# Optimization experiments

Measured on AMD Instinct MI355X. Metric: run time of the kernel, lower is better.

Reference implementation:

```python
import jax, jax.numpy as jnp
import numpy as np


def setup_inputs() -> dict:
    key = jax.random.key(0)
    k1, k2 = jax.random.split(key)
    B, Q, K, H = 8, 2048, 2048, 128
    out_state = jax.random.normal(k1, (B, Q, H), dtype=jnp.float32)
    history = jax.random.normal(k2, (B, K, H), dtype=jnp.float32)
    return {"out_state": out_state, "history": history}


def reference(out_state, history):
    # tanh pre-activation on queries
    q = jnp.tanh(out_state)                              # [B, Q, H]
    # unscaled QK^T scores
    scores = jnp.einsum("bqh,bkh->bqk", q, history)      # [B, Q, K]
    probs = jax.nn.softmax(scores, axis=2)               # softmax over keys
    attn = jnp.einsum("bqk,bkh->bqh", probs, history)    # [B, Q, H]
    return attn
```

## Files before the change

### kernel.cpp

```cpp
#include <hip/hip_runtime.h>
#include <math.h>


typedef _Float16 half8 __attribute__((ext_vector_type(8)));
typedef _Float16 half4 __attribute__((ext_vector_type(4)));
typedef float    f32x4 __attribute__((ext_vector_type(4)));

#define QQ 2048
#define KK 2048
#define HH 128
#define BM 128
#define BN 64
#define NTILES 32
#define NGROUPS 128
#define KS_STR 132
#define VT_STR 68
#define PS_STR 66
#define L2E 1.44269504f
#define SPLITS_MAX 6
#define OSPLIT  ((size_t)NGROUPS * BM * HH)
#define MLSPLIT ((size_t)NGROUPS * BM)

union U32H { unsigned int u; _Float16 h[2]; };

__launch_bounds__(256, 3)
__global__ void attn_main(const float* __restrict__ out_state,
                          const float* __restrict__ history,
                          float* __restrict__ out,
                          float* __restrict__ ws,
                          int splits) {
    __shared__ _Float16 Ks[BN * KS_STR];
    __shared__ _Float16 Vt[HH * VT_STR];
    __shared__ _Float16 Ps[4][2][16 * PS_STR];

    const int tid  = threadIdx.x;
    const int wave = tid >> 6;
    const int lane = tid & 63;
    const int quad = lane >> 4;
    const int lc   = lane & 15;

    const int bid = blockIdx.x;
    const int b   = bid & 7;
    const int t   = bid >> 3;
    const int qb  = t & 15;
    const int s   = t >> 4;
    const int g   = b * 16 + qb;
    const int m0  = qb * BM;

    const int kt0 = (NTILES * s) / splits;
    const int kt1 = (NTILES * (s + 1)) / splits;

    half8 qfa[4], qfb[4];
    {
        const float* qrowA = out_state + ((size_t)b * QQ + m0 + wave * 32 + lc) * HH;
        const float* qrowB = qrowA + 16 * HH;
        #pragma unroll
        for (int s4 = 0; s4 < 4; ++s4) {
            const int h0 = 32 * s4 + quad * 8;
            float4 a = *(const float4*)(qrowA + h0);
            float4 c = *(const float4*)(qrowA + h0 + 4);
            qfa[s4][0] = (_Float16)tanhf(a.x); qfa[s4][1] = (_Float16)tanhf(a.y);
            qfa[s4][2] = (_Float16)tanhf(a.z); qfa[s4][3] = (_Float16)tanhf(a.w);
            qfa[s4][4] = (_Float16)tanhf(c.x); qfa[s4][5] = (_Float16)tanhf(c.y);
            qfa[s4][6] = (_Float16)tanhf(c.z); qfa[s4][7] = (_Float16)tanhf(c.w);
            a = *(const float4*)(qrowB + h0);
            c = *(const float4*)(qrowB + h0 + 4);
            qfb[s4][0] = (_Float16)tanhf(a.x); qfb[s4][1] = (_Float16)tanhf(a.y);
            qfb[s4][2] = (_Float16)tanhf(a.z); qfb[s4][3] = (_Float16)tanhf(a.w);
            qfb[s4][4] = (_Float16)tanhf(c.x); qfb[s4][5] = (_Float16)tanhf(c.y);
            qfb[s4][6] = (_Float16)tanhf(c.z); qfb[s4][7] = (_Float16)tanhf(c.w);
        }
    }

    const f32x4 zero4 = {0.f, 0.f, 0.f, 0.f};
    f32x4 Oa[8], Ob[8];
    #pragma unroll
    for (int i = 0; i < 8; ++i) { Oa[i] = zero4; Ob[i] = zero4; }
    f32x4 OsumA = zero4, OsumB = zero4;
    float rmaxA = -3.0e38f, rmaxB = -3.0e38f;

    const int r0  = tid >> 5;
    const int c4  = (tid & 31) * 4;
    const int h0  = 2 * (tid & 63);
    const int n0t = (tid >> 6) * 16;

    const half8 ones = {(_Float16)1.f,(_Float16)1.f,(_Float16)1.f,(_Float16)1.f,
                        (_Float16)1.f,(_Float16)1.f,(_Float16)1.f,(_Float16)1.f};

    for (int kt = kt0; kt < kt1; ++kt) {
        const int n0 = kt * BN;

        float4 gbuf[8];
        const float* hb = history + ((size_t)b * KK + n0) * HH;
        #pragma unroll
        for (int j = 0; j < 8; ++j)
            gbuf[j] = *(const float4*)(hb + (size_t)(r0 + 8 * j) * HH + c4);

        __syncthreads();
        #pragma unroll
        for (int j = 0; j < 8; ++j) {
            half4 hv;
            hv[0] = (_Float16)gbuf[j].x; hv[1] = (_Float16)gbuf[j].y;
            hv[2] = (_Float16)gbuf[j].z; hv[3] = (_Float16)gbuf[j].w;
            *(half4*)&Ks[(r0 + 8 * j) * KS_STR + c4] = hv;
        }
        __syncthreads();
        {
            half8 ra0, ra1, rb0, rb1;
            #pragma unroll
            for (int i = 0; i < 8; ++i) {
                U32H t2; t2.u = *(const unsigned int*)&Ks[(n0t + i) * KS_STR + h0];
                ra0[i] = t2.h[0]; rb0[i] = t2.h[1];
            }
            #pragma unroll
            for (int i = 8; i < 16; ++i) {
                U32H t2; t2.u = *(const unsigned int*)&Ks[(n0t + i) * KS_STR + h0];
                ra1[i - 8] = t2.h[0]; rb1[i - 8] = t2.h[1];
            }
            *(half8*)&Vt[(h0    ) * VT_STR + n0t    ] = ra0;
            *(half8*)&Vt[(h0    ) * VT_STR + n0t + 8] = ra1;
            *(half8*)&Vt[(h0 + 1) * VT_STR + n0t    ] = rb0;
            *(half8*)&Vt[(h0 + 1) * VT_STR + n0t + 8] = rb1;
        }
        __syncthreads();

        f32x4 Sa[4], Sb[4];
        #pragma unroll
        for (int nt = 0; nt < 4; ++nt) {
            f32x4 aa = zero4, ab = zero4;
            #pragma unroll
            for (int s4 = 0; s4 < 4; ++s4) {
                half8 kf = *(half8*)&Ks[(nt * 16 + lc) * KS_STR + 32 * s4 + quad * 8];
                aa = __builtin_amdgcn_mfma_f32_16x16x32_f16(kf, qfa[s4], aa, 0, 0, 0);
                ab = __builtin_amdgcn_mfma_f32_16x16x32_f16(kf, qfb[s4], ab, 0, 0, 0);
            }
            Sa[nt] = aa; Sb[nt] = ab;
        }

        float tmaxA = Sa[0][0], tmaxB = Sb[0][0];
        #pragma unroll
        for (int nt = 0; nt < 4; ++nt)
            #pragma unroll
            for (int r = 0; r < 4; ++r) {
                tmaxA = fmaxf(tmaxA, Sa[nt][r]);
                tmaxB = fmaxf(tmaxB, Sb[nt][r]);
            }
        tmaxA = fmaxf(tmaxA, __shfl_xor(tmaxA, 16, 64));
        tmaxA = fmaxf(tmaxA, __shfl_xor(tmaxA, 32, 64));
        tmaxB = fmaxf(tmaxB, __shfl_xor(tmaxB, 16, 64));
        tmaxB = fmaxf(tmaxB, __shfl_xor(tmaxB, 32, 64));

        const float nmA = fmaxf(rmaxA, tmaxA);
        const float nmB = fmaxf(rmaxB, tmaxB);
        const float alphaA = exp2f((rmaxA - nmA) * L2E);
        const float alphaB = exp2f((rmaxB - nmB) * L2E);
        rmaxA = nmA; rmaxB = nmB;

        #pragma unroll
        for (int nt = 0; nt < 4; ++nt)
            #pragma unroll
            for (int r = 0; r < 4; ++r) {
                Sa[nt][r] = exp2f((Sa[nt][r] - nmA) * L2E);
                Sb[nt][r] = exp2f((Sb[nt][r] - nmB) * L2E);
            }

        #pragma unroll
        for (int ct = 0; ct < 8; ++ct) { Oa[ct] *= alphaA; Ob[ct] *= alphaB; }
        OsumA *= alphaA; OsumB *= alphaB;

        #pragma unroll
        for (int nt = 0; nt < 4; ++nt) {
            half4 pva, pvb;
            pva[0] = (_Float16)Sa[nt][0]; pva[1] = (_Float16)Sa[nt][1];
            pva[2] = (_Float16)Sa[nt][2]; pva[3] = (_Float16)Sa[nt][3];
            pvb[0] = (_Float16)Sb[nt][0]; pvb[1] = (_Float16)Sb[nt][1];
            pvb[2] = (_Float16)Sb[nt][2]; pvb[3] = (_Float16)Sb[nt][3];
            *(half4*)&Ps[wave][0][lc * PS_STR + nt * 16 + quad * 4] = pva;
            *(half4*)&Ps[wave][1][lc * PS_STR + nt * 16 + quad * 4] = pvb;
        }

        #pragma unroll
        for (int s2 = 0; s2 < 2; ++s2) {
            half8 pba = *(half8*)&Ps[wave][0][lc * PS_STR + s2 * 32 + quad * 8];
            half8 pbb = *(half8*)&Ps[wave][1][lc * PS_STR + s2 * 32 + quad * 8];
            OsumA = __builtin_amdgcn_mfma_f32_16x16x32_f16(ones, pba, OsumA, 0, 0, 0);
            OsumB = __builtin_amdgcn_mfma_f32_16x16x32_f16(ones, pbb, OsumB, 0, 0, 0);
            #pragma unroll
            for (int ct = 0; ct < 8; ++ct) {
                half8 vf = *(half8*)&Vt[(ct * 16 + lc) * VT_STR + s2 * 32 + quad * 8];
                Oa[ct] = __builtin_amdgcn_mfma_f32_16x16x32_f16(vf, pba, Oa[ct], 0, 0, 0);
                Ob[ct] = __builtin_amdgcn_mfma_f32_16x16x32_f16(vf, pbb, Ob[ct], 0, 0, 0);
            }
        }
    }

    const int qA = wave * 32 + lc;
    if (splits == 1) {
        const float invA = 1.0f / OsumA[0];
        const float invB = 1.0f / OsumB[0];
        float* orowA = out + ((size_t)b * QQ + m0 + qA) * HH;
        float* orowB = orowA + 16 * HH;
        #pragma unroll
        for (int ct = 0; ct < 8; ++ct) {
            f32x4 va = Oa[ct] * invA;
            f32x4 vb = Ob[ct] * invB;
            *(f32x4*)&orowA[ct * 16 + quad * 4] = va;
            *(f32x4*)&orowB[ct * 16 + quad * 4] = vb;
        }
        return;
    }

    const size_t mBase = (size_t)splits * OSPLIT;
    const size_t lBase = mBase + (size_t)splits * MLSPLIT;
    float* poA = ws + ((size_t)s * NGROUPS + g) * ((size_t)BM * HH) + (size_t)qA * HH;
    float* poB = poA + 16 * HH;
    #pragma unroll
    for (int ct = 0; ct < 8; ++ct) {
        *(f32x4*)&poA[ct * 16 + quad * 4] = Oa[ct];
        *(f32x4*)&poB[ct * 16 + quad * 4] = Ob[ct];
    }
    if (quad == 0) {
        const size_t idx = (size_t)(s * NGROUPS + g) * BM + qA;
        ws[mBase + idx]      = rmaxA;
        ws[lBase + idx]      = OsumA[0];
        ws[mBase + idx + 16] = rmaxB;
        ws[lBase + idx + 16] = OsumB[0];
    }
}

__global__ void attn_combine(const float* __restrict__ ws,
                             float* __restrict__ out,
                             int splits) {
    const int idx = blockIdx.x * 256 + threadIdx.x;
    const int h4   = (idx & 31) * 4;
    const int rest = idx >> 5;
    const int q    = rest & 2047;
    const int b    = rest >> 11;
    const int g    = b * 16 + (q >> 7);
    const int qr   = q & 127;

    const size_t mBase = (size_t)splits * OSPLIT;
    const size_t lBase = mBase + (size_t)splits * MLSPLIT;

    float ms[SPLITS_MAX];
    float M = -3.0e38f;
    for (int sp = 0; sp < splits; ++sp) {
        ms[sp] = ws[mBase + (size_t)(sp * NGROUPS + g) * BM + qr];
        M = fmaxf(M, ms[sp]);
    }
    float denom = 0.f;
    f32x4 val = {0.f, 0.f, 0.f, 0.f};
    for (int sp = 0; sp < splits; ++sp) {
        const float w = exp2f((ms[sp] - M) * L2E);
        denom += w * ws[lBase + (size_t)(sp * NGROUPS + g) * BM + qr];
        const f32x4 ov = *(const f32x4*)&ws[(size_t)(sp * NGROUPS + g) * ((size_t)BM * HH)
                                            + (size_t)qr * HH + h4];
        val += w * ov;
    }
    const float inv = 1.0f / denom;
    *(f32x4*)&out[((size_t)b * QQ + q) * HH + h4] = val * inv;
}

extern "C" void kernel_launch(void* const* d_in, const int* in_sizes, int n_in,
                              void* d_out, int out_size, void* d_ws, size_t ws_size,
                              hipStream_t stream) {
    const float* out_state = (const float*)d_in[0];
    const float* history   = (const float*)d_in[1];
    float* out = (float*)d_out;
    float* ws  = (float*)d_ws;

    int splits = 1;
    for (int cand = SPLITS_MAX; cand >= 2; --cand) {
        const size_t bytes = (size_t)cand * (OSPLIT + 2 * MLSPLIT) * 4;
        if (ws_size >= bytes) { splits = cand; break; }
    }

    attn_main<<<dim3(NGROUPS * splits), dim3(256), 0, stream>>>(out_state, history, out, ws, splits);
    if (splits > 1)
        attn_combine<<<dim3((8 * QQ * HH / 4) / 256), dim3(256), 0, stream>>>(ws, out, splits);
}
```

Before: 118.7 us.

## Keep P in registers via 16x16x16 MFMA, fold log2e into Q, fp16 split partials

Switches the PV product to 16x16x16 MFMAs whose B-operand layout matches the QK accumulator, so probabilities go straight from registers to MFMA and the per-wave Ps shared-memory round trip is gone. log2e is folded into the tanh'd queries, removing the per-score multiply before exp2. Split partial outputs are stored in fp16 to halve workspace traffic, max splits rise to 8, the launch-bounds occupancy hint goes to 4, and the combine kernel's indexing is remapped. The costs are twice as many, smaller MFMAs, more register pressure under the tighter occupancy bound, and extra fp16 rounding of the partial outputs.

Result: slower. 180.3 us (+51.9%).

```diff
diff --git a/kernel.cpp b/kernel.cpp
--- a/kernel.cpp
+++ b/kernel.cpp
@@ -15,23 +15,21 @@
 #define NGROUPS 128
 #define KS_STR 132
 #define VT_STR 68
-#define PS_STR 66
 #define L2E 1.44269504f
-#define SPLITS_MAX 6
+#define SPLITS_MAX 8
 #define OSPLIT  ((size_t)NGROUPS * BM * HH)
 #define MLSPLIT ((size_t)NGROUPS * BM)
 
 union U32H { unsigned int u; _Float16 h[2]; };
 
-__launch_bounds__(256, 3)
+__launch_bounds__(256, 4)
 __global__ void attn_main(const float* __restrict__ out_state,
                           const float* __restrict__ history,
                           float* __restrict__ out,
-                          float* __restrict__ ws,
+                          void* __restrict__ wsv,
                           int splits) {
     __shared__ _Float16 Ks[BN * KS_STR];
     __shared__ _Float16 Vt[HH * VT_STR];
-    __shared__ _Float16 Ps[4][2][16 * PS_STR];
 
     const int tid  = threadIdx.x;
     const int wave = tid >> 6;
@@ -59,16 +57,16 @@
             const int h0 = 32 * s4 + quad * 8;
             float4 a = *(const float4*)(qrowA + h0);
             float4 c = *(const float4*)(qrowA + h0 + 4);
-            qfa[s4][0] = (_Float16)tanhf(a.x); qfa[s4][1] = (_Float16)tanhf(a.y);
-            qfa[s4][2] = (_Float16)tanhf(a.z); qfa[s4][3] = (_Float16)tanhf(a.w);
-            qfa[s4][4] = (_Float16)tanhf(c.x); qfa[s4][5] = (_Float16)tanhf(c.y);
-            qfa[s4][6] = (_Float16)tanhf(c.z); qfa[s4][7] = (_Float16)tanhf(c.w);
+            qfa[s4][0] = (_Float16)(L2E * tanhf(a.x)); qfa[s4][1] = (_Float16)(L2E * tanhf(a.y));
+            qfa[s4][2] = (_Float16)(L2E * tanhf(a.z)); qfa[s4][3] = (_Float16)(L2E * tanhf(a.w));
+            qfa[s4][4] = (_Float16)(L2E * tanhf(c.x)); qfa[s4][5] = (_Float16)(L2E * tanhf(c.y));
+            qfa[s4][6] = (_Float16)(L2E * tanhf(c.z)); qfa[s4][7] = (_Float16)(L2E * tanhf(c.w));
             a = *(const float4*)(qrowB + h0);
             c = *(const float4*)(qrowB + h0 + 4);
-            qfb[s4][0] = (_Float16)tanhf(a.x); qfb[s4][1] = (_Float16)tanhf(a.y);
-            qfb[s4][2] = (_Float16)tanhf(a.z); qfb[s4][3] = (_Float16)tanhf(a.w);
-            qfb[s4][4] = (_Float16)tanhf(c.x); qfb[s4][5] = (_Float16)tanhf(c.y);
-            qfb[s4][6] = (_Float16)tanhf(c.z); qfb[s4][7] = (_Float16)tanhf(c.w);
+            qfb[s4][0] = (_Float16)(L2E * tanhf(a.x)); qfb[s4][1] = (_Float16)(L2E * tanhf(a.y));
+            qfb[s4][2] = (_Float16)(L2E * tanhf(a.z)); qfb[s4][3] = (_Float16)(L2E * tanhf(a.w));
+            qfb[s4][4] = (_Float16)(L2E * tanhf(c.x)); qfb[s4][5] = (_Float16)(L2E * tanhf(c.y));
+            qfb[s4][6] = (_Float16)(L2E * tanhf(c.z)); qfb[s4][7] = (_Float16)(L2E * tanhf(c.w));
         }
     }
 
@@ -84,8 +82,7 @@
     const int h0  = 2 * (tid & 63);
     const int n0t = (tid >> 6) * 16;
 
-    const half8 ones = {(_Float16)1.f,(_Float16)1.f,(_Float16)1.f,(_Float16)1.f,
-                        (_Float16)1.f,(_Float16)1.f,(_Float16)1.f,(_Float16)1.f};
+    const half4 ones4 = {(_Float16)1.f, (_Float16)1.f, (_Float16)1.f, (_Float16)1.f};
 
     for (int kt = kt0; kt < kt1; ++kt) {
         const int n0 = kt * BN;
@@ -152,17 +149,9 @@
 
         const float nmA = fmaxf(rmaxA, tmaxA);
         const float nmB = fmaxf(rmaxB, tmaxB);
-        const float alphaA = exp2f((rmaxA - nmA) * L2E);
-        const float alphaB = exp2f((rmaxB - nmB) * L2E);
+        const float alphaA = exp2f(rmaxA - nmA);
+        const float alphaB = exp2f(rmaxB - nmB);
         rmaxA = nmA; rmaxB = nmB;
-
-        #pragma unroll
-        for (int nt = 0; nt < 4; ++nt)
-            #pragma unroll
-            for (int r = 0; r < 4; ++r) {
-                Sa[nt][r] = exp2f((Sa[nt][r] - nmA) * L2E);
-                Sb[nt][r] = exp2f((Sb[nt][r] - nmB) * L2E);
-            }
 
         #pragma unroll
         for (int ct = 0; ct < 8; ++ct) { Oa[ct] *= alphaA; Ob[ct] *= alphaB; }
@@ -170,26 +159,19 @@
 
         #pragma unroll
         for (int nt = 0; nt < 4; ++nt) {
-            half4 pva, pvb;
-            pva[0] = (_Float16)Sa[nt][0]; pva[1] = (_Float16)Sa[nt][1];
-            pva[2] = (_Float16)Sa[nt][2]; pva[3] = (_Float16)Sa[nt][3];
-            pvb[0] = (_Float16)Sb[nt][0]; pvb[1] = (_Float16)Sb[nt][1];
-            pvb[2] = (_Float16)Sb[nt][2]; pvb[3] = (_Float16)Sb[nt][3];
-            *(half4*)&Ps[wave][0][lc * PS_STR + nt * 16 + quad * 4] = pva;
-            *(half4*)&Ps[wave][1][lc * PS_STR + nt * 16 + quad * 4] = pvb;
-        }
-
-        #pragma unroll
-        for (int s2 = 0; s2 < 2; ++s2) {
-            half8 pba = *(half8*)&Ps[wave][0][lc * PS_STR + s2 * 32 + quad * 8];
-            half8 pbb = *(half8*)&Ps[wave][1][lc * PS_STR + s2 * 32 + quad * 8];
-            OsumA = __builtin_amdgcn_mfma_f32_16x16x32_f16(ones, pba, OsumA, 0, 0, 0);
-            OsumB = __builtin_amdgcn_mfma_f32_16x16x32_f16(ones, pbb, OsumB, 0, 0, 0);
+            half4 pba, pbb;
+            #pragma unroll
+            for (int r = 0; r < 4; ++r) {
+                pba[r] = (_Float16)exp2f(Sa[nt][r] - nmA);
+                pbb[r] = (_Float16)exp2f(Sb[nt][r] - nmB);
+            }
+            OsumA = __builtin_amdgcn_mfma_f32_16x16x16f16(ones4, pba, OsumA, 0, 0, 0);
+            OsumB = __builtin_amdgcn_mfma_f32_16x16x16f16(ones4, pbb, OsumB, 0, 0, 0);
             #pragma unroll
             for (int ct = 0; ct < 8; ++ct) {
-                half8 vf = *(half8*)&Vt[(ct * 16 + lc) * VT_STR + s2 * 32 + quad * 8];
-                Oa[ct] = __builtin_amdgcn_mfma_f32_16x16x32_f16(vf, pba, Oa[ct], 0, 0, 0);
-                Ob[ct] = __builtin_amdgcn_mfma_f32_16x16x32_f16(vf, pbb, Ob[ct], 0, 0, 0);
+                half4 va = *(half4*)&Vt[(ct * 16 + lc) * VT_STR + nt * 16 + quad * 4];
+                Oa[ct] = __builtin_amdgcn_mfma_f32_16x16x16f16(va, pba, Oa[ct], 0, 0, 0);
+                Ob[ct] = __builtin_amdgcn_mfma_f32_16x16x16f16(va, pbb, Ob[ct], 0, 0, 0);
             }
         }
     }
@@ -210,52 +192,58 @@
         return;
     }
 
-    const size_t mBase = (size_t)splits * OSPLIT;
-    const size_t lBase = mBase + (size_t)splits * MLSPLIT;
-    float* poA = ws + ((size_t)s * NGROUPS + g) * ((size_t)BM * HH) + (size_t)qA * HH;
-    float* poB = poA + 16 * HH;
+    _Float16* wsO = (_Float16*)wsv;
+    float*    wsM = (float*)((char*)wsv + (size_t)splits * OSPLIT * 2);
+    float*    wsL = wsM + (size_t)splits * MLSPLIT;
+
+    _Float16* poA = wsO + ((size_t)s * NGROUPS + g) * ((size_t)BM * HH) + (size_t)qA * HH;
+    _Float16* poB = poA + 16 * HH;
     #pragma unroll
     for (int ct = 0; ct < 8; ++ct) {
-        *(f32x4*)&poA[ct * 16 + quad * 4] = Oa[ct];
-        *(f32x4*)&poB[ct * 16 + quad * 4] = Ob[ct];
+        half4 ha, hb2;
+        #pragma unroll
+        for (int r = 0; r < 4; ++r) { ha[r] = (_Float16)Oa[ct][r]; hb2[r] = (_Float16)Ob[ct][r]; }
+        *(half4*)&poA[ct * 16 + quad * 4] = ha;
+        *(half4*)&poB[ct * 16 + quad * 4] = hb2;
     }
     if (quad == 0) {
         const size_t idx = (size_t)(s * NGROUPS + g) * BM + qA;
-        ws[mBase + idx]      = rmaxA;
-        ws[lBase + idx]      = OsumA[0];
-        ws[mBase + idx + 16] = rmaxB;
-        ws[lBase + idx + 16] = OsumB[0];
+        wsM[idx]      = rmaxA;
+        wsL[idx]      = OsumA[0];
+        wsM[idx + 16] = rmaxB;
+        wsL[idx + 16] = OsumB[0];
     }
 }
 
-__global__ void attn_combine(const float* __restrict__ ws,
+__global__ void attn_combine(const void* __restrict__ wsv,
                              float* __restrict__ out,
                              int splits) {
-    const int idx = blockIdx.x * 256 + threadIdx.x;
-    const int h4   = (idx & 31) * 4;
-    const int rest = idx >> 5;
-    const int q    = rest & 2047;
-    const int b    = rest >> 11;
-    const int g    = b * 16 + (q >> 7);
-    const int qr   = q & 127;
-
-    const size_t mBase = (size_t)splits * OSPLIT;
-    const size_t lBase = mBase + (size_t)splits * MLSPLIT;
+    const int b      = blockIdx.x & 7;
+    const int qchunk = blockIdx.x >> 3;
+    const int h4 = (threadIdx.x & 31) * 4;
+    const int q  = qchunk * 8 + (threadIdx.x >> 5);
+    const int g  = b * 16 + (q >> 7);
+    const int qr = q & 127;
+
+    const _Float16* wsO = (const _Float16*)wsv;
+    const float*    wsM = (const float*)((const char*)wsv + (size_t)splits * OSPLIT * 2);
+    const float*    wsL = wsM + (size_t)splits * MLSPLIT;
 
     float ms[SPLITS_MAX];
     float M = -3.0e38f;
     for (int sp = 0; sp < splits; ++sp) {
-        ms[sp] = ws[mBase + (size_t)(sp * NGROUPS + g) * BM + qr];
+        ms[sp] = wsM[(size_t)(sp * NGROUPS + g) * BM + qr];
         M = fmaxf(M, ms[sp]);
     }
     float denom = 0.f;
     f32x4 val = {0.f, 0.f, 0.f, 0.f};
     for (int sp = 0; sp < splits; ++sp) {
-        const float w = exp2f((ms[sp] - M) * L2E);
-        denom += w * ws[lBase + (size_t)(sp * NGROUPS + g) * BM + qr];
-        const f32x4 ov = *(const f32x4*)&ws[(size_t)(sp * NGROUPS + g) * ((size_t)BM * HH)
-                                            + (size_t)qr * HH + h4];
-        val += w * ov;
+        const float w = exp2f(ms[sp] - M);
+        denom += w * wsL[(size_t)(sp * NGROUPS + g) * BM + qr];
+        const half4 ov = *(const half4*)&wsO[(size_t)(sp * NGROUPS + g) * ((size_t)BM * HH)
+                                             + (size_t)qr * HH + h4];
+        #pragma unroll
+        for (int i = 0; i < 4; ++i) val[i] += w * (float)ov[i];
     }
     const float inv = 1.0f / denom;
     *(f32x4*)&out[((size_t)b * QQ + q) * HH + h4] = val * inv;
@@ -267,15 +255,15 @@
     const float* out_state = (const float*)d_in[0];
     const float* history   = (const float*)d_in[1];
     float* out = (float*)d_out;
-    float* ws  = (float*)d_ws;
 
     int splits = 1;
-    for (int cand = SPLITS_MAX; cand >= 2; --cand) {
-        const size_t bytes = (size_t)cand * (OSPLIT + 2 * MLSPLIT) * 4;
-        if (ws_size >= bytes) { splits = cand; break; }
-    }
-
-    attn_main<<<dim3(NGROUPS * splits), dim3(256), 0, stream>>>(out_state, history, out, ws, splits);
+    const int cands[5] = {8, 6, 4, 3, 2};
+    for (int i = 0; i < 5; ++i) {
+        const size_t bytes = (size_t)cands[i] * (OSPLIT * 2 + 2 * MLSPLIT * 4);
+        if (ws_size >= bytes) { splits = cands[i]; break; }
+    }
+
+    attn_main<<<dim3(NGROUPS * splits), dim3(256), 0, stream>>>(out_state, history, out, d_ws, splits);
     if (splits > 1)
-        attn_combine<<<dim3((8 * QQ * HH / 4) / 256), dim3(256), 0, stream>>>(ws, out, splits);
+        attn_combine<<<dim3(2048), dim3(256), 0, stream>>>(d_ws, out, splits);
 }
```
